# Performance work log

Measured on AMD Instinct MI355X. Metric: run time of the kernel, lower is better.

Reference implementation:

```python
import jax, jax.numpy as jnp
import numpy as np

B, T = 8, 16384
CLASSES, RC, EC = 256, 32, 256
NLAYERS = 40          # blocks(4) * layers(10)
DIL = 1024            # source uses 2**layers for every layer (faithful to code)
EPS = 1e-5


def _shift_right(x, d):
    # causal shift: y[t] = x[t-d], zero-padded
    return jnp.pad(x, ((0, 0), (0, 0), (d, 0)))[:, :, : x.shape[-1]]


def _conv1x1(x, w, b):
    # w: [out, in], x: [B, in, T]
    return jnp.einsum('oi,bit->bot', w, x) + b[None, :, None]


def _dconv2(x, w, b, d):
    # causal dilated conv, kernel 2: y[t] = w[:,:,0] x[t-d] + w[:,:,1] x[t] + b
    return (jnp.einsum('oi,bit->bot', w[:, :, 1], x)
            + jnp.einsum('oi,bit->bot', w[:, :, 0], _shift_right(x, d))
            + b[None, :, None])


def _bn(x, g, b):
    # training-mode BatchNorm1d: batch stats over (N, L)
    m = jnp.mean(x, axis=(0, 2), keepdims=True)
    v = jnp.var(x, axis=(0, 2), keepdims=True)
    return (x - m) * jax.lax.rsqrt(v + EPS) * g[None, :, None] + b[None, :, None]


def _mish(x):
    return x * jnp.tanh(jax.nn.softplus(x))


def setup_inputs() -> dict:
    key = jax.random.key(0)
    ks = jax.random.split(key, 16)
    n = jax.random.normal
    return {
        'x': n(ks[0], (B, CLASSES, T), jnp.float32),
        'start_w': n(ks[1], (RC, CLASSES), jnp.float32) * 0.05,
        'start_b': n(ks[2], (RC,), jnp.float32) * 0.05,
        'gt_w': n(ks[3], (NLAYERS, RC, RC, 2), jnp.float32) * 0.1,   # tanh branch
        'gt_b': n(ks[4], (NLAYERS, RC), jnp.float32) * 0.05,
        'gs_w': n(ks[5], (NLAYERS, RC, RC, 2), jnp.float32) * 0.1,   # sigmoid branch
        'gs_b': n(ks[6], (NLAYERS, RC), jnp.float32) * 0.05,
        'res_w': n(ks[7], (NLAYERS, RC, RC), jnp.float32) * 0.1,
        'res_b': n(ks[8], (NLAYERS, RC), jnp.float32) * 0.05,
        'bn_g': jnp.ones((NLAYERS, RC), jnp.float32),
        'bn_b': jnp.zeros((NLAYERS, RC), jnp.float32),
        'bn1_g': jnp.ones((RC,), jnp.float32),
        'bn1_b': jnp.zeros((RC,), jnp.float32),
        'e1_w': n(ks[9], (EC, RC), jnp.float32) * 0.1,
        'e1_b': n(ks[10], (EC,), jnp.float32) * 0.05,
        'bn2_g': jnp.ones((EC,), jnp.float32),
        'bn2_b': jnp.zeros((EC,), jnp.float32),
        'e2_w': n(ks[11], (CLASSES, EC), jnp.float32) * 0.05,
        'e2_b': n(ks[12], (CLASSES,), jnp.float32) * 0.05,
    }


def reference(x, start_w, start_b, gt_w, gt_b, gs_w, gs_b, res_w, res_b,
              bn_g, bn_b, bn1_g, bn1_b, e1_w, e1_b, bn2_g, bn2_b, e2_w, e2_b):
    # start_conv: CausalConv(classes, RC, k=1, shift=1) -> 1x1 conv on x shifted right by 1
    h = _conv1x1(_shift_right(x, 1), start_w, start_b)  # [B, RC, T]

    def step(carry, p):
        h, skip = carry
        gtw, gtb, gsw, gsb, rw, rb, bg, bb = p
        g = jnp.tanh(_dconv2(h, gtw, gtb, DIL)) * jax.nn.sigmoid(_dconv2(h, gsw, gsb, DIL))
        skip = skip + g
        h = h + _bn(_conv1x1(g, rw, rb), bg, bb)
        return (h, skip), None

    init = (h, jnp.zeros_like(h))
    (h, skip_sum), _ = jax.lax.scan(
        step, init, (gt_w, gt_b, gs_w, gs_b, res_w, res_b, bn_g, bn_b))

    y = _mish(_bn(skip_sum, bn1_g, bn1_b))
    y = _mish(_bn(_conv1x1(y, e1_w, e1_b), bn2_g, bn2_b))
    return _conv1x1(y, e2_w, e2_b)  # [B, CLASSES, T]
```

## Files before the change

kernel.cpp:

```cpp
#include <hip/hip_runtime.h>
#include <hip/hip_cooperative_groups.h>

namespace cg = cooperative_groups;


#define EPSV 1e-5f
#define RN   (1.f/131072.f)

#define H_OFF  0
#define SK_OFF (4*1024*1024)
#define ST_OFF (8*1024*1024)
#define ST_SKIP 2560
#define ST_MU   2624
#define ST_Y    2656
#define ST_A2   3680
#define ST_B2   3936
#define ST_TOT  4192
#define LST_N   (40*8*64)

__device__ __forceinline__ float rcp_f(float x) { return __builtin_amdgcn_rcpf(x); }
__device__ __forceinline__ float tanh_f(float x) {
    float e = __expf(2.f * x);
    return 1.f - 2.f * rcp_f(e + 1.f);
}
__device__ __forceinline__ float sigm_f(float x) { return rcp_f(1.f + __expf(-x)); }
__device__ __forceinline__ float mish_f(float x) {
    float e = __expf(x);
    float sp = (x > 15.f) ? x : __logf(1.f + e);
    return x * tanh_f(sp);
}

__global__ void k_zero(float* __restrict__ p, int n) {
    int i = blockIdx.x * 256 + threadIdx.x;
    if (i < n) p[i] = 0.f;
}

__global__ __launch_bounds__(256) void k_start(
        const float* __restrict__ x, const float* __restrict__ sw_g,
        const float* __restrict__ sb_g, float* __restrict__ h, float* __restrict__ skip)
{
    __shared__ float sw[256*36];
    __shared__ float sb[32];
    int tid = threadIdx.x, blk = blockIdx.x;
    int b = blk >> 6, r0 = (blk & 63) << 4;
    for (int k = tid; k < 8192; k += 256) {
        int o = k >> 8, c = k & 255;
        sw[c*36 + o] = sw_g[k];
    }
    if (tid < 32) sb[tid] = sb_g[tid];
    __syncthreads();

    int rr = tid & 15, s = tid >> 4;
    int t = r0 + rr + (s << 10);
    bool valid = (t >= 1);
    const float* xr = x + (long)b*256*16384 + (valid ? (t-1) : 0);
    float acc[32];
    #pragma unroll
    for (int o = 0; o < 32; ++o) acc[o] = 0.f;
    for (int c = 0; c < 256; ++c) {
        float xv = xr[(long)c*16384];
        xv = valid ? xv : 0.f;
        const float4* wrow = (const float4*)&sw[c*36];
        #pragma unroll
        for (int o4 = 0; o4 < 8; ++o4) {
            float4 w = wrow[o4];
            acc[o4*4+0] += w.x*xv; acc[o4*4+1] += w.y*xv;
            acc[o4*4+2] += w.z*xv; acc[o4*4+3] += w.w*xv;
        }
    }
    __syncthreads();
    #pragma unroll
    for (int o = 0; o < 32; ++o) sw[(rr*32 + o)*16 + s] = acc[o] + sb[o];
    __syncthreads();
    float4* hd = (float4*)(h + (long)blk*8192);
    float4* sd = (float4*)(skip + (long)blk*8192);
    const float4* ss = (const float4*)sw;
    float4 z4 = make_float4(0.f, 0.f, 0.f, 0.f);
    for (int k = tid; k < 2048; k += 256) { hd[k] = ss[k]; sd[k] = z4; }
}

__global__ __launch_bounds__(512, 4) void k_fused(
        const float* __restrict__ gt_w, const float* __restrict__ gt_b,
        const float* __restrict__ gs_w, const float* __restrict__ gs_b,
        const float* __restrict__ res_w, const float* __restrict__ res_b,
        const float* __restrict__ bn_g, const float* __restrict__ bn_b,
        const float* __restrict__ h, float* __restrict__ skip,
        float* __restrict__ st, float* __restrict__ lst)
{
    __shared__ float s_w[4096];
    __shared__ float s_r[1024];
    __shared__ float s_hg[8192];
    __shared__ float s_red[8][32][2];
    __shared__ float s_ab[64];

    int tid = threadIdx.x;
    int o = tid & 31, chl = tid >> 5;
    long base = (long)blockIdx.x*8192 + chl*512 + o*16;
    int slot = blockIdx.x & 7;

    float hreg[16], sk[16], zr[16];
    {
        const float4* hp4 = (const float4*)(h + base);
        #pragma unroll
        for (int q = 0; q < 4; ++q) {
            float4 t4 = hp4[q];
            hreg[4*q+0]=t4.x; hreg[4*q+1]=t4.y; hreg[4*q+2]=t4.z; hreg[4*q+3]=t4.w;
        }
    }
    #pragma unroll
    for (int s = 0; s < 16; ++s) sk[s] = 0.f;

    cg::grid_group grid = cg::this_grid();

    for (int L = 0; L < 40; ++L) {
        for (int k = tid; k < 1024; k += 512) {
            int oo = k >> 5, ii = k & 31;
            float2 a = ((const float2*)(gt_w + (long)L*2048))[k];
            float2 c = ((const float2*)(gs_w + (long)L*2048))[k];
            float* d = &s_w[(ii*32 + oo)*4];
            d[0] = a.x; d[1] = a.y; d[2] = c.x; d[3] = c.y;
            s_r[ii*32 + oo] = res_w[(long)L*1024 + k];
        }

        if (L > 0) {
            if (tid < 32) {
                float ssum = 0.f, ssq = 0.f;
                #pragma unroll
                for (int r = 0; r < 8; ++r) {
                    ssum += __hip_atomic_load(&lst[((L-1)*8 + r)*64 + tid],
                                              __ATOMIC_RELAXED, __HIP_MEMORY_SCOPE_AGENT);
                    ssq  += __hip_atomic_load(&lst[((L-1)*8 + r)*64 + 32 + tid],
                                              __ATOMIC_RELAXED, __HIP_MEMORY_SCOPE_AGENT);
                }
                float m = ssum * RN;
                float v = ssq * RN - m*m;
                float a = rsqrtf(v + EPSV) * bn_g[(L-1)*32 + tid];
                s_ab[tid] = a;
                s_ab[32 + tid] = bn_b[(L-1)*32 + tid] - m*a;
            }
            __syncthreads();
            float a = s_ab[o], bb = s_ab[32 + o];
            #pragma unroll
            for (int s = 0; s < 16; ++s) hreg[s] += zr[s]*a + bb;
        }

        float4* hs4 = (float4*)&s_hg[chl*512 + o*16];
        #pragma unroll
        for (int q = 0; q < 4; ++q)
            hs4[q] = make_float4(hreg[4*q], hreg[4*q+1], hreg[4*q+2], hreg[4*q+3]);
        __syncthreads();

        float aT[16], aS[16];
        float gtb = gt_b[L*32 + o], gsb = gs_b[L*32 + o];
        #pragma unroll
        for (int s = 0; s < 16; ++s) { aT[s] = gtb; aS[s] = gsb; }
        #pragma unroll 4
        for (int i = 0; i < 32; ++i) {
            float4 w = *(const float4*)&s_w[(i*32 + o)*4];
            const float4* hr = (const float4*)&s_hg[chl*512 + i*16];
            float hp = 0.f;
            #pragma unroll
            for (int s4 = 0; s4 < 4; ++s4) {
                float4 hv = hr[s4];
                int s = 4*s4;
                aT[s+0] += w.y*hv.x + w.x*hp;   aS[s+0] += w.w*hv.x + w.z*hp;
                aT[s+1] += w.y*hv.y + w.x*hv.x; aS[s+1] += w.w*hv.y + w.z*hv.x;
                aT[s+2] += w.y*hv.z + w.x*hv.y; aS[s+2] += w.w*hv.z + w.z*hv.y;
                aT[s+3] += w.y*hv.w + w.x*hv.z; aS[s+3] += w.w*hv.w + w.z*hv.z;
                hp = hv.w;
            }
        }
        float g[16];
        #pragma unroll
        for (int s = 0; s < 16; ++s) {
            g[s] = tanh_f(aT[s]) * sigm_f(aS[s]);
            sk[s] += g[s];
        }

        if (L < 39) {
            __syncthreads();
            #pragma unroll
            for (int q = 0; q < 4; ++q)
                hs4[q] = make_float4(g[4*q], g[4*q+1], g[4*q+2], g[4*q+3]);
            __syncthreads();

            float rbv = res_b[L*32 + o];
            #pragma unroll
            for (int s = 0; s < 16; ++s) zr[s] = rbv;
            #pragma unroll 4
            for (int i = 0; i < 32; ++i) {
                float w = s_r[i*32 + o];
                const float4* gr = (const float4*)&s_hg[chl*512 + i*16];
                #pragma unroll
                for (int s4 = 0; s4 < 4; ++s4) {
                    float4 gv = gr[s4];
                    zr[4*s4+0] += w*gv.x; zr[4*s4+1] += w*gv.y;
                    zr[4*s4+2] += w*gv.z; zr[4*s4+3] += w*gv.w;
                }
            }

            float ps = 0.f, pq = 0.f;
            #pragma unroll
            for (int s = 0; s < 16; ++s) { ps += zr[s]; pq += zr[s]*zr[s]; }
            ps += __shfl_down(ps, 32); pq += __shfl_down(pq, 32);
            int wv = tid >> 6;
            if ((tid & 63) < 32) { s_red[wv][o][0] = ps; s_red[wv][o][1] = pq; }
            __syncthreads();
            if (tid < 32) {
                float a = 0.f;
                #pragma unroll
                for (int w8 = 0; w8 < 8; ++w8) a += s_red[w8][tid][0];
                atomicAdd(&lst[(L*8 + slot)*64 + tid], a);
            } else if (tid < 64) {
                int c = tid - 32;
                float a = 0.f;
                #pragma unroll
                for (int w8 = 0; w8 < 8; ++w8) a += s_red[w8][c][1];
                atomicAdd(&lst[(L*8 + slot)*64 + 32 + c], a);
            }
            grid.sync();
        }
    }

    {
        float4* skp4 = (float4*)(skip + base);
        #pragma unroll
        for (int q = 0; q < 4; ++q)
            skp4[q] = make_float4(sk[4*q], sk[4*q+1], sk[4*q+2], sk[4*q+3]);

        float p2 = 0.f, q2 = 0.f;
        #pragma unroll
        for (int s = 0; s < 16; ++s) { p2 += sk[s]; q2 += sk[s]*sk[s]; }
        p2 += __shfl_down(p2, 32); q2 += __shfl_down(q2, 32);
        int wv = tid >> 6;
        __syncthreads();
        if ((tid & 63) < 32) { s_red[wv][o][0] = p2; s_red[wv][o][1] = q2; }
        __syncthreads();
        if (tid < 32) {
            float a = 0.f;
            #pragma unroll
            for (int w8 = 0; w8 < 8; ++w8) a += s_red[w8][tid][0];
            atomicAdd(&st[ST_SKIP + tid], a);
        } else if (tid < 64) {
            int c = tid - 32;
            float a = 0.f;
            #pragma unroll
            for (int w8 = 0; w8 < 8; ++w8) a += s_red[w8][c][1];
            atomicAdd(&st[ST_SKIP + 32 + c], a);
        }
    }
}

__global__ __launch_bounds__(256) void k_layer(
        const float* __restrict__ gt_w, const float* __restrict__ gt_b,
        const float* __restrict__ gs_w, const float* __restrict__ gs_b,
        const float* __restrict__ res_w, const float* __restrict__ res_b,
        const float* __restrict__ bn_g, const float* __restrict__ bn_b,
        float* __restrict__ h, float* __restrict__ z, float* __restrict__ skip,
        float* __restrict__ st, int L)
{
    __shared__ float s_w[4096];
    __shared__ float s_r[1024];
    __shared__ float s_hg[4096];
    __shared__ float s_red[4][32][2];

    int tid = threadIdx.x;
    int o = tid & 31, chl = tid >> 5;
    long base = (long)blockIdx.x*4096 + chl*512 + o*16;

    for (int k = tid; k < 1024; k += 256) {
        int oo = k >> 5, ii = k & 31;
        float2 a = ((const float2*)(gt_w + (long)L*2048))[k];
        float2 c = ((const float2*)(gs_w + (long)L*2048))[k];
        float* d = &s_w[(ii*32 + oo)*4];
        d[0] = a.x; d[1] = a.y; d[2] = c.x; d[3] = c.y;
        s_r[ii*32 + oo] = res_w[(long)L*1024 + k];
    }

    float hreg[16];
    float4* hp4 = (float4*)(h + base);
    #pragma unroll
    for (int q = 0; q < 4; ++q) {
        float4 t4 = hp4[q];
        hreg[4*q+0]=t4.x; hreg[4*q+1]=t4.y; hreg[4*q+2]=t4.z; hreg[4*q+3]=t4.w;
    }
    if (L > 0) {
        float ssum = st[(L-1)*64 + o], ssq = st[(L-1)*64 + 32 + o];
        float m = ssum * RN;
        float v = ssq * RN - m*m;
        float a = rsqrtf(v + EPSV) * bn_g[(L-1)*32 + o];
        float bb = bn_b[(L-1)*32 + o] - m*a;
        const float4* zp4 = (const float4*)(z + base);
        #pragma unroll
        for (int q = 0; q < 4; ++q) {
            float4 t4 = zp4[q];
            hreg[4*q+0] += t4.x*a + bb; hreg[4*q+1] += t4.y*a + bb;
            hreg[4*q+2] += t4.z*a + bb; hreg[4*q+3] += t4.w*a + bb;
        }
        #pragma unroll
        for (int q = 0; q < 4; ++q)
            hp4[q] = make_float4(hreg[4*q], hreg[4*q+1], hreg[4*q+2], hreg[4*q+3]);
    }
    float4* hs4 = (float4*)&s_hg[chl*512 + o*16];
    #pragma unroll
    for (int q = 0; q < 4; ++q)
        hs4[q] = make_float4(hreg[4*q], hreg[4*q+1], hreg[4*q+2], hreg[4*q+3]);
    __syncthreads();

    float aT[16], aS[16];
    float gtb = gt_b[L*32 + o], gsb = gs_b[L*32 + o];
    #pragma unroll
    for (int s = 0; s < 16; ++s) { aT[s] = gtb; aS[s] = gsb; }
    #pragma unroll 4
    for (int i = 0; i < 32; ++i) {
        float4 w = *(const float4*)&s_w[(i*32 + o)*4];
        const float4* hr = (const float4*)&s_hg[chl*512 + i*16];
        float hp = 0.f;
        #pragma unroll
        for (int s4 = 0; s4 < 4; ++s4) {
            float4 hv = hr[s4];
            int s = 4*s4;
            aT[s+0] += w.y*hv.x + w.x*hp;   aS[s+0] += w.w*hv.x + w.z*hp;
            aT[s+1] += w.y*hv.y + w.x*hv.x; aS[s+1] += w.w*hv.y + w.z*hv.x;
            aT[s+2] += w.y*hv.z + w.x*hv.y; aS[s+2] += w.w*hv.z + w.z*hv.y;
            aT[s+3] += w.y*hv.w + w.x*hv.z; aS[s+3] += w.w*hv.w + w.z*hv.z;
            hp = hv.w;
        }
    }
    float g[16], sk[16];
    #pragma unroll
    for (int s = 0; s < 16; ++s) g[s] = tanh_f(aT[s]) * sigm_f(aS[s]);

    float4* skp4 = (float4*)(skip + base);
    #pragma unroll
    for (int q = 0; q < 4; ++q) {
        float4 t4 = skp4[q];
        sk[4*q+0] = t4.x + g[4*q+0]; sk[4*q+1] = t4.y + g[4*q+1];
        sk[4*q+2] = t4.z + g[4*q+2]; sk[4*q+3] = t4.w + g[4*q+3];
        skp4[q] = make_float4(sk[4*q], sk[4*q+1], sk[4*q+2], sk[4*q+3]);
    }

    __syncthreads();
    #pragma unroll
    for (int q = 0; q < 4; ++q)
        hs4[q] = make_float4(g[4*q], g[4*q+1], g[4*q+2], g[4*q+3]);
    __syncthreads();

    float az[16];
    float rbv = res_b[L*32 + o];
    #pragma unroll
    for (int s = 0; s < 16; ++s) az[s] = rbv;
    #pragma unroll 4
    for (int i = 0; i < 32; ++i) {
        float w = s_r[i*32 + o];
        const float4* gr = (const float4*)&s_hg[chl*512 + i*16];
        #pragma unroll
        for (int s4 = 0; s4 < 4; ++s4) {
            float4 gv = gr[s4];
            az[4*s4+0] += w*gv.x; az[4*s4+1] += w*gv.y;
            az[4*s4+2] += w*gv.z; az[4*s4+3] += w*gv.w;
        }
    }
    float4* zp4w = (float4*)(z + base);
    #pragma unroll
    for (int q = 0; q < 4; ++q)
        zp4w[q] = make_float4(az[4*q], az[4*q+1], az[4*q+2], az[4*q+3]);

    float ps = 0.f, pq = 0.f;
    #pragma unroll
    for (int s = 0; s < 16; ++s) { ps += az[s]; pq += az[s]*az[s]; }
    ps += __shfl_down(ps, 32); pq += __shfl_down(pq, 32);
    int wv = tid >> 6;
    if ((tid & 63) < 32) { s_red[wv][o][0] = ps; s_red[wv][o][1] = pq; }
    __syncthreads();
    if (tid < 32) {
        float a = s_red[0][tid][0] + s_red[1][tid][0] + s_red[2][tid][0] + s_red[3][tid][0];
        atomicAdd(&st[L*64 + tid], a);
    } else if (tid < 64) {
        int c = tid - 32;
        float a = s_red[0][c][1] + s_red[1][c][1] + s_red[2][c][1] + s_red[3][c][1];
        atomicAdd(&st[L*64 + 32 + c], a);
    }

    if (L == 39) {
        float p2 = 0.f, q2 = 0.f;
        #pragma unroll
        for (int s = 0; s < 16; ++s) { p2 += sk[s]; q2 += sk[s]*sk[s]; }
        p2 += __shfl_down(p2, 32); q2 += __shfl_down(q2, 32);
        __syncthreads();
        if ((tid & 63) < 32) { s_red[wv][o][0] = p2; s_red[wv][o][1] = q2; }
        __syncthreads();
        if (tid < 32) {
            float a = s_red[0][tid][0] + s_red[1][tid][0] + s_red[2][tid][0] + s_red[3][tid][0];
            atomicAdd(&st[ST_SKIP + tid], a);
        } else if (tid < 64) {
            int c = tid - 32;
            float a = s_red[0][c][1] + s_red[1][c][1] + s_red[2][c][1] + s_red[3][c][1];
            atomicAdd(&st[ST_SKIP + 32 + c], a);
        }
    }
}

__global__ __launch_bounds__(256) void k_ep_a(
        const float* __restrict__ skip, const float* __restrict__ bn1_g,
        const float* __restrict__ bn1_b, float* __restrict__ st)
{
    __shared__ float sy[256*33];
    __shared__ float sA[32], sB[32];
    int tid = threadIdx.x;
    long cb = (long)blockIdx.x * 8192;
    if (tid < 32) {
        float ssum = st[ST_SKIP + tid], ssq = st[ST_SKIP + 32 + tid];
        float m = ssum * RN, v = ssq * RN - m*m;
        float a = rsqrtf(v + EPSV) * bn1_g[tid];
        sA[tid] = a; sB[tid] = bn1_b[tid] - m*a;
    }
    __syncthreads();
    for (int k = tid; k < 8192; k += 256) {
        int i = k & 31, p = k >> 5;
        int rr = p & 15, s = p >> 4;
        float v = skip[cb + rr*512 + i*16 + s];
        sy[p*33 + i] = mish_f(v * sA[i] + sB[i]);
    }
    __syncthreads();
    if (tid < 32) {
        float mu = 0.f;
        for (int p = 0; p < 256; ++p) mu += sy[p*33 + tid];
        atomicAdd(&st[ST_MU + tid], mu);
    }
    int jj = tid & 31, i0 = tid >> 5;
    float a0 = 0.f, a1 = 0.f, a2 = 0.f, a3 = 0.f;
    for (int p = 0; p < 256; ++p) {
        float yj = sy[p*33 + jj];
        a0 += yj * sy[p*33 + i0];
        a1 += yj * sy[p*33 + i0 + 8];
        a2 += yj * sy[p*33 + i0 + 16];
        a3 += yj * sy[p*33 + i0 + 24];
    }
    atomicAdd(&st[ST_Y + (i0     )*32 + jj], a0);
    atomicAdd(&st[ST_Y + (i0 +  8)*32 + jj], a1);
    atomicAdd(&st[ST_Y + (i0 + 16)*32 + jj], a2);
    atomicAdd(&st[ST_Y + (i0 + 24)*32 + jj], a3);
}

__global__ void k_ep_b(
        const float* __restrict__ e1_w, const float* __restrict__ e1_b,
        const float* __restrict__ bn2_g, const float* __restrict__ bn2_b,
        float* __restrict__ st)
{
    __shared__ float mu[32];
    int o = threadIdx.x;
    if (o < 32) mu[o] = st[ST_MU + o] * RN;
    __syncthreads();
    float w[32];
    const float4* wr = (const float4*)(e1_w + o*32);
    #pragma unroll
    for (int q = 0; q < 8; ++q) {
        float4 t4 = wr[q];
        w[4*q]=t4.x; w[4*q+1]=t4.y; w[4*q+2]=t4.z; w[4*q+3]=t4.w;
    }
    float m2 = e1_b[o];
    #pragma unroll
    for (int i = 0; i < 32; ++i) m2 += w[i]*mu[i];
    float var = 0.f;
    for (int i = 0; i < 32; ++i) {
        float wi = w[i], mi = mu[i];
        for (int j = 0; j < 32; ++j)
            var += wi * w[j] * (st[ST_Y + i*32 + j]*RN - mi*mu[j]);
    }
    float a2 = rsqrtf(var + EPSV) * bn2_g[o];
    st[ST_A2 + o] = a2;
    st[ST_B2 + o] = bn2_b[o] - m2*a2;
}

__global__ __launch_bounds__(256, 4) void k_ep_c(
        const float* __restrict__ skip,
        const float* __restrict__ bn1_g, const float* __restrict__ bn1_b,
        const float* __restrict__ e1_w, const float* __restrict__ e1_b,
        const float* __restrict__ e2_w, const float* __restrict__ e2_b,
        const float* __restrict__ st, float* __restrict__ out)
{
    __shared__ float y1l[32*32];
    __shared__ float y2l[256*36];
    int tid = threadIdx.x;
    int blk2 = blockIdx.x;
    int blk = blk2 >> 1, half = blk2 & 1;
    int b = blk >> 6, r0 = (blk & 63) << 4;
    long cb = (long)blk * 8192;
    float w1[32];
    {
        const float4* wr = (const float4*)(e1_w + tid*32);
        #pragma unroll
        for (int q = 0; q < 8; ++q) {
            float4 t4 = wr[q];
            w1[4*q]=t4.x; w1[4*q+1]=t4.y; w1[4*q+2]=t4.z; w1[4*q+3]=t4.w;
        }
    }
    float a2 = st[ST_A2 + tid], b2 = st[ST_B2 + tid];
    float eb1 = e1_b[tid];
    float eb2 = e2_b[tid];
    const float4* w2row = (const float4*)(e2_w + (long)tid * 256);

    for (int st8 = half*4; st8 < half*4 + 4; ++st8) {
        for (int k = tid; k < 1024; k += 256) {
            int i = k >> 5, q = k & 31;
            float ssum = st[ST_SKIP + i], ssq = st[ST_SKIP + 32 + i];
            float m = ssum * RN, vv = ssq * RN - m*m;
            float a1 = rsqrtf(vv + EPSV) * bn1_g[i];
            float b1 = bn1_b[i] - m*a1;
            int rr = q & 15, sl = q >> 4;
            float v = skip[cb + rr*512 + i*16 + st8*2 + sl];
            y1l[i*32 + q] = mish_f(v * a1 + b1);
        }
        __syncthreads();
        #pragma unroll 2
        for (int q4 = 0; q4 < 8; ++q4) {
            float4 acc = make_float4(eb1, eb1, eb1, eb1);
            #pragma unroll 8
            for (int i = 0; i < 32; ++i) {
                float4 yv = *(const float4*)&y1l[i*32 + q4*4];
                float wi = w1[i];
                acc.x += wi*yv.x; acc.y += wi*yv.y; acc.z += wi*yv.z; acc.w += wi*yv.w;
            }
            float4 y2v;
            y2v.x = mish_f(acc.x*a2 + b2);
            y2v.y = mish_f(acc.y*a2 + b2);
            y2v.z = mish_f(acc.z*a2 + b2);
            y2v.w = mish_f(acc.w*a2 + b2);
            *(float4*)&y2l[tid*36 + q4*4] = y2v;
        }
        __syncthreads();
        float acc[32];
        #pragma unroll
        for (int q = 0; q < 32; ++q) acc[q] = eb2;
        for (int i4 = 0; i4 < 64; ++i4) {
            float4 w4 = w2row[i4];
            float wa[4] = {w4.x, w4.y, w4.z, w4.w};
            #pragma unroll
            for (int ii = 0; ii < 4; ++ii) {
                float wv = wa[ii];
                const float* yr = &y2l[(i4*4 + ii)*36];
                #pragma unroll
                for (int q4 = 0; q4 < 8; ++q4) {
                    float4 yv = *(const float4*)&yr[q4*4];
                    acc[q4*4+0] += wv*yv.x; acc[q4*4+1] += wv*yv.y;
                    acc[q4*4+2] += wv*yv.z; acc[q4*4+3] += wv*yv.w;
                }
            }
        }
        long ob = ((long)b*256 + tid)*16384 + (long)(st8*2)*1024 + r0;
        float4* op = (float4*)&out[ob];
        op[0] = make_float4(acc[0],  acc[1],  acc[2],  acc[3]);
        op[1] = make_float4(acc[4],  acc[5],  acc[6],  acc[7]);
        op[2] = make_float4(acc[8],  acc[9],  acc[10], acc[11]);
        op[3] = make_float4(acc[12], acc[13], acc[14], acc[15]);
        float4* op2 = (float4*)&out[ob + 1024];
        op2[0] = make_float4(acc[16], acc[17], acc[18], acc[19]);
        op2[1] = make_float4(acc[20], acc[21], acc[22], acc[23]);
        op2[2] = make_float4(acc[24], acc[25], acc[26], acc[27]);
        op2[3] = make_float4(acc[28], acc[29], acc[30], acc[31]);
    }
}

extern "C" void kernel_launch(void* const* d_in, const int* in_sizes, int n_in,
                              void* d_out, int out_size, void* d_ws, size_t ws_size,
                              hipStream_t stream) {
    const float* x       = (const float*)d_in[0];
    const float* start_w = (const float*)d_in[1];
    const float* start_b = (const float*)d_in[2];
    const float* gt_w    = (const float*)d_in[3];
    const float* gt_b    = (const float*)d_in[4];
    const float* gs_w    = (const float*)d_in[5];
    const float* gs_b    = (const float*)d_in[6];
    const float* res_w   = (const float*)d_in[7];
    const float* res_b   = (const float*)d_in[8];
    const float* bn_g    = (const float*)d_in[9];
    const float* bn_b    = (const float*)d_in[10];
    const float* bn1_g   = (const float*)d_in[11];
    const float* bn1_b   = (const float*)d_in[12];
    const float* e1_w    = (const float*)d_in[13];
    const float* e1_b    = (const float*)d_in[14];
    const float* bn2_g   = (const float*)d_in[15];
    const float* bn2_b   = (const float*)d_in[16];
    const float* e2_w    = (const float*)d_in[17];
    const float* e2_b    = (const float*)d_in[18];
    float* ws  = (float*)d_ws;
    float* out = (float*)d_out;

    float* h    = ws + H_OFF;
    float* skip = ws + SK_OFF;
    float* st   = ws + ST_OFF;
    float* lst  = out;

    int coop_ok = 0;
    {
        int dev = 0, attr = 0, occ = 0;
        if (hipGetDevice(&dev) == hipSuccess &&
            hipDeviceGetAttribute(&attr, hipDeviceAttributeCooperativeLaunch, dev)
                == hipSuccess && attr) {
            if (hipOccupancyMaxActiveBlocksPerMultiprocessor(&occ, k_fused, 512, 0)
                    == hipSuccess && occ >= 2)
                coop_ok = 1;
        }
    }

    k_zero<<<dim3(17), dim3(256), 0, stream>>>(st, ST_TOT);
    k_zero<<<dim3(80), dim3(256), 0, stream>>>(lst, LST_N);
    k_start<<<dim3(512), dim3(256), 0, stream>>>(x, start_w, start_b, h, skip);

    if (coop_ok) {
        void* kargs[12] = {
            (void*)&gt_w, (void*)&gt_b, (void*)&gs_w, (void*)&gs_b,
            (void*)&res_w, (void*)&res_b, (void*)&bn_g, (void*)&bn_b,
            (void*)&h, (void*)&skip, (void*)&st, (void*)&lst };
        if (hipLaunchCooperativeKernel(k_fused, dim3(512), dim3(512),
                                       kargs, 0, stream) != hipSuccess)
            coop_ok = 0;
    }
    if (!coop_ok) {
        size_t need_full = ((size_t)ST_OFF + 8192 + 4*1024*1024) * 4;
        float* z = (ws_size >= need_full) ? (ws + ST_OFF + 8192)
                                          : (float*)d_out;
        for (int L = 0; L < 40; ++L)
            k_layer<<<dim3(1024), dim3(256), 0, stream>>>(
                gt_w, gt_b, gs_w, gs_b, res_w, res_b, bn_g, bn_b, h, z, skip, st, L);
    }

    k_ep_a<<<dim3(512), dim3(256), 0, stream>>>(skip, bn1_g, bn1_b, st);
    k_ep_b<<<dim3(1), dim3(256), 0, stream>>>(e1_w, e1_b, bn2_g, bn2_b, st);
    k_ep_c<<<dim3(1024), dim3(256), 0, stream>>>(skip, bn1_g, bn1_b, e1_w, e1_b,
                                                 e2_w, e2_b, st, out);
}
```

Baseline: 2.611 ms.

## Coarsen fused WaveNet kernel to two chunks per thread with swizzled LDS rows

```diff
diff --git a/kernel.cpp b/kernel.cpp
--- a/kernel.cpp
+++ b/kernel.cpp
@@ -79,7 +79,62 @@
     for (int k = tid; k < 2048; k += 256) { hd[k] = ss[k]; sd[k] = z4; }
 }
 
-__global__ __launch_bounds__(512, 4) void k_fused(
+__device__ __forceinline__ void stage16(float* __restrict__ row, int o,
+                                        const float* __restrict__ v) {
+    float4* p = (float4*)row;
+    int sw = (o >> 1) & 3;
+    p[0^sw] = make_float4(v[0],  v[1],  v[2],  v[3]);
+    p[1^sw] = make_float4(v[4],  v[5],  v[6],  v[7]);
+    p[2^sw] = make_float4(v[8],  v[9],  v[10], v[11]);
+    p[3^sw] = make_float4(v[12], v[13], v[14], v[15]);
+}
+
+__device__ __forceinline__ void gate_mv(const float* __restrict__ s_w,
+        const float* __restrict__ hg, int o, float gtb, float gsb,
+        float* __restrict__ aT, float* __restrict__ aS)
+{
+    #pragma unroll
+    for (int s = 0; s < 16; ++s) { aT[s] = gtb; aS[s] = gsb; }
+    #pragma unroll 4
+    for (int i = 0; i < 32; ++i) {
+        float4 w = *(const float4*)&s_w[(i*32 + o)*4];
+        const float4* hr = (const float4*)&hg[i*16];
+        int swi = (i >> 1) & 3;
+        float hv[16];
+        *(float4*)&hv[0]  = hr[0^swi];
+        *(float4*)&hv[4]  = hr[1^swi];
+        *(float4*)&hv[8]  = hr[2^swi];
+        *(float4*)&hv[12] = hr[3^swi];
+        aT[0] += w.y*hv[0];  aS[0] += w.w*hv[0];
+        #pragma unroll
+        for (int s = 1; s < 16; ++s) {
+            aT[s] += w.y*hv[s] + w.x*hv[s-1];
+            aS[s] += w.w*hv[s] + w.z*hv[s-1];
+        }
+    }
+}
+
+__device__ __forceinline__ void res_mv(const float* __restrict__ s_r,
+        const float* __restrict__ hg, int o, float rbv, float* __restrict__ zr)
+{
+    #pragma unroll
+    for (int s = 0; s < 16; ++s) zr[s] = rbv;
+    #pragma unroll 4
+    for (int i = 0; i < 32; ++i) {
+        float w = s_r[i*32 + o];
+        const float4* gr = (const float4*)&hg[i*16];
+        int swi = (i >> 1) & 3;
+        float gv[16];
+        *(float4*)&gv[0]  = gr[0^swi];
+        *(float4*)&gv[4]  = gr[1^swi];
+        *(float4*)&gv[8]  = gr[2^swi];
+        *(float4*)&gv[12] = gr[3^swi];
+        #pragma unroll
+        for (int s = 0; s < 16; ++s) zr[s] += w*gv[s];
+    }
+}
+
+__global__ __launch_bounds__(256, 2) void k_fused2(
         const float* __restrict__ gt_w, const float* __restrict__ gt_b,
         const float* __restrict__ gs_w, const float* __restrict__ gs_b,
         const float* __restrict__ res_w, const float* __restrict__ res_b,
@@ -90,30 +145,35 @@
     __shared__ float s_w[4096];
     __shared__ float s_r[1024];
     __shared__ float s_hg[8192];
-    __shared__ float s_red[8][32][2];
+    __shared__ float s_red[4][32][2];
     __shared__ float s_ab[64];
 
     int tid = threadIdx.x;
-    int o = tid & 31, chl = tid >> 5;
-    long base = (long)blockIdx.x*8192 + chl*512 + o*16;
+    int o = tid & 31, c0 = tid >> 5;
+    long baseA = (long)blockIdx.x*8192 + c0*512 + o*16;
+    long baseB = baseA + 8*512;
     int slot = blockIdx.x & 7;
-
-    float hreg[16], sk[16], zr[16];
+    float* rowA = &s_hg[c0*512 + o*16];
+    float* rowB = &s_hg[(c0+8)*512 + o*16];
+
+    float hA[16], hB[16], skA[16], skB[16], zrA[16], zrB[16];
     {
-        const float4* hp4 = (const float4*)(h + base);
+        const float4* pa = (const float4*)(h + baseA);
+        const float4* pb = (const float4*)(h + baseB);
         #pragma unroll
         for (int q = 0; q < 4; ++q) {
-            float4 t4 = hp4[q];
-            hreg[4*q+0]=t4.x; hreg[4*q+1]=t4.y; hreg[4*q+2]=t4.z; hreg[4*q+3]=t4.w;
-        }
-    }
-    #pragma unroll
-    for (int s = 0; s < 16; ++s) sk[s] = 0.f;
+            float4 ta = pa[q], tb = pb[q];
+            hA[4*q+0]=ta.x; hA[4*q+1]=ta.y; hA[4*q+2]=ta.z; hA[4*q+3]=ta.w;
+            hB[4*q+0]=tb.x; hB[4*q+1]=tb.y; hB[4*q+2]=tb.z; hB[4*q+3]=tb.w;
+        }
+    }
+    #pragma unroll
+    for (int s = 0; s < 16; ++s) { skA[s] = 0.f; skB[s] = 0.f; }
 
     cg::grid_group grid = cg::this_grid();
 
     for (int L = 0; L < 40; ++L) {
-        for (int k = tid; k < 1024; k += 512) {
+        for (int k = tid; k < 1024; k += 256) {
             int oo = k >> 5, ii = k & 31;
             float2 a = ((const float2*)(gt_w + (long)L*2048))[k];
             float2 c = ((const float2*)(gs_w + (long)L*2048))[k];
@@ -121,101 +181,78 @@
             d[0] = a.x; d[1] = a.y; d[2] = c.x; d[3] = c.y;
             s_r[ii*32 + oo] = res_w[(long)L*1024 + k];
         }
+        if (L > 0 && tid < 32) {
+            float ssum = 0.f, ssq = 0.f;
+            #pragma unroll
+            for (int r = 0; r < 8; ++r) {
+                ssum += __hip_atomic_load(&lst[((L-1)*8 + r)*64 + tid],
+                                          __ATOMIC_RELAXED, __HIP_MEMORY_SCOPE_AGENT);
+                ssq  += __hip_atomic_load(&lst[((L-1)*8 + r)*64 + 32 + tid],
+                                          __ATOMIC_RELAXED, __HIP_MEMORY_SCOPE_AGENT);
+            }
+            float m = ssum * RN;
+            float v = ssq * RN - m*m;
+            float a = rsqrtf(v + EPSV) * bn_g[(L-1)*32 + tid];
+            s_ab[tid] = a;
+            s_ab[32 + tid] = bn_b[(L-1)*32 + tid] - m*a;
+        }
+        __syncthreads();
 
         if (L > 0) {
-            if (tid < 32) {
-                float ssum = 0.f, ssq = 0.f;
-                #pragma unroll
-                for (int r = 0; r < 8; ++r) {
-                    ssum += __hip_atomic_load(&lst[((L-1)*8 + r)*64 + tid],
-                                              __ATOMIC_RELAXED, __HIP_MEMORY_SCOPE_AGENT);
-                    ssq  += __hip_atomic_load(&lst[((L-1)*8 + r)*64 + 32 + tid],
-                                              __ATOMIC_RELAXED, __HIP_MEMORY_SCOPE_AGENT);
-                }
-                float m = ssum * RN;
-                float v = ssq * RN - m*m;
-                float a = rsqrtf(v + EPSV) * bn_g[(L-1)*32 + tid];
-                s_ab[tid] = a;
-                s_ab[32 + tid] = bn_b[(L-1)*32 + tid] - m*a;
-            }
-            __syncthreads();
             float a = s_ab[o], bb = s_ab[32 + o];
             #pragma unroll
-            for (int s = 0; s < 16; ++s) hreg[s] += zr[s]*a + bb;
-        }
-
-        float4* hs4 = (float4*)&s_hg[chl*512 + o*16];
-        #pragma unroll
-        for (int q = 0; q < 4; ++q)
-            hs4[q] = make_float4(hreg[4*q], hreg[4*q+1], hreg[4*q+2], hreg[4*q+3]);
-        __syncthreads();
-
-        float aT[16], aS[16];
-        float gtb = gt_b[L*32 + o], gsb = gs_b[L*32 + o];
-        #pragma unroll
-        for (int s = 0; s < 16; ++s) { aT[s] = gtb; aS[s] = gsb; }
-        #pragma unroll 4
-        for (int i = 0; i < 32; ++i) {
-            float4 w = *(const float4*)&s_w[(i*32 + o)*4];
-            const float4* hr = (const float4*)&s_hg[chl*512 + i*16];
-            float hp = 0.f;
+            for (int s = 0; s < 16; ++s) {
+                hA[s] += zrA[s]*a + bb;
+                hB[s] += zrB[s]*a + bb;
+            }
+        }
+
+        stage16(rowA, o, hA);
+        stage16(rowB, o, hB);
+
+        float gA[16], gB[16];
+        {
+            float aT[16], aS[16];
+            float gtb = gt_b[L*32 + o], gsb = gs_b[L*32 + o];
+            gate_mv(s_w, &s_hg[c0*512], o, gtb, gsb, aT, aS);
             #pragma unroll
-            for (int s4 = 0; s4 < 4; ++s4) {
-                float4 hv = hr[s4];
-                int s = 4*s4;
-                aT[s+0] += w.y*hv.x + w.x*hp;   aS[s+0] += w.w*hv.x + w.z*hp;
-                aT[s+1] += w.y*hv.y + w.x*hv.x; aS[s+1] += w.w*hv.y + w.z*hv.x;
-                aT[s+2] += w.y*hv.z + w.x*hv.y; aS[s+2] += w.w*hv.z + w.z*hv.y;
-                aT[s+3] += w.y*hv.w + w.x*hv.z; aS[s+3] += w.w*hv.w + w.z*hv.z;
-                hp = hv.w;
-            }
-        }
-        float g[16];
-        #pragma unroll
-        for (int s = 0; s < 16; ++s) {
-            g[s] = tanh_f(aT[s]) * sigm_f(aS[s]);
-            sk[s] += g[s];
+            for (int s = 0; s < 16; ++s) {
+                gA[s] = tanh_f(aT[s]) * sigm_f(aS[s]);
+                skA[s] += gA[s];
+            }
+            gate_mv(s_w, &s_hg[(c0+8)*512], o, gtb, gsb, aT, aS);
+            #pragma unroll
+            for (int s = 0; s < 16; ++s) {
+                gB[s] = tanh_f(aT[s]) * sigm_f(aS[s]);
+                skB[s] += gB[s];
+            }
         }
 
         if (L < 39) {
-            __syncthreads();
-            #pragma unroll
-            for (int q = 0; q < 4; ++q)
-                hs4[q] = make_float4(g[4*q], g[4*q+1], g[4*q+2], g[4*q+3]);
-            __syncthreads();
-
+            stage16(rowA, o, gA);
+            stage16(rowB, o, gB);
             float rbv = res_b[L*32 + o];
-            #pragma unroll
-            for (int s = 0; s < 16; ++s) zr[s] = rbv;
-            #pragma unroll 4
-            for (int i = 0; i < 32; ++i) {
-                float w = s_r[i*32 + o];
-                const float4* gr = (const float4*)&s_hg[chl*512 + i*16];
-                #pragma unroll
-                for (int s4 = 0; s4 < 4; ++s4) {
-                    float4 gv = gr[s4];
-                    zr[4*s4+0] += w*gv.x; zr[4*s4+1] += w*gv.y;
-                    zr[4*s4+2] += w*gv.z; zr[4*s4+3] += w*gv.w;
-                }
-            }
+            res_mv(s_r, &s_hg[c0*512],     o, rbv, zrA);
+            res_mv(s_r, &s_hg[(c0+8)*512], o, rbv, zrB);
 
             float ps = 0.f, pq = 0.f;
             #pragma unroll
-            for (int s = 0; s < 16; ++s) { ps += zr[s]; pq += zr[s]*zr[s]; }
+            for (int s = 0; s < 16; ++s) {
+                ps += zrA[s] + zrB[s];
+                pq += zrA[s]*zrA[s] + zrB[s]*zrB[s];
+            }
             ps += __shfl_down(ps, 32); pq += __shfl_down(pq, 32);
             int wv = tid >> 6;
             if ((tid & 63) < 32) { s_red[wv][o][0] = ps; s_red[wv][o][1] = pq; }
             __syncthreads();
             if (tid < 32) {
-                float a = 0.f;
-                #pragma unroll
-                for (int w8 = 0; w8 < 8; ++w8) a += s_red[w8][tid][0];
+                float a = s_red[0][tid][0] + s_red[1][tid][0]
+                        + s_red[2][tid][0] + s_red[3][tid][0];
                 atomicAdd(&lst[(L*8 + slot)*64 + tid], a);
             } else if (tid < 64) {
                 int c = tid - 32;
-                float a = 0.f;
-                #pragma unroll
-                for (int w8 = 0; w8 < 8; ++w8) a += s_red[w8][c][1];
+                float a = s_red[0][c][1] + s_red[1][c][1]
+                        + s_red[2][c][1] + s_red[3][c][1];
                 atomicAdd(&lst[(L*8 + slot)*64 + 32 + c], a);
             }
             grid.sync();
@@ -223,29 +260,31 @@
     }
 
     {
-        float4* skp4 = (float4*)(skip + base);
-        #pragma unroll
-        for (int q = 0; q < 4; ++q)
-            skp4[q] = make_float4(sk[4*q], sk[4*q+1], sk[4*q+2], sk[4*q+3]);
-
+        float4* pa = (float4*)(skip + baseA);
+        float4* pb = (float4*)(skip + baseB);
+        #pragma unroll
+        for (int q = 0; q < 4; ++q) {
+            pa[q] = make_float4(skA[4*q], skA[4*q+1], skA[4*q+2], skA[4*q+3]);
+            pb[q] = make_float4(skB[4*q], skB[4*q+1], skB[4*q+2], skB[4*q+3]);
+        }
         float p2 = 0.f, q2 = 0.f;
         #pragma unroll
-        for (int s = 0; s < 16; ++s) { p2 += sk[s]; q2 += sk[s]*sk[s]; }
+        for (int s = 0; s < 16; ++s) {
+            p2 += skA[s] + skB[s];
+            q2 += skA[s]*skA[s] + skB[s]*skB[s];
+        }
         p2 += __shfl_down(p2, 32); q2 += __shfl_down(q2, 32);
         int wv = tid >> 6;
-        __syncthreads();
         if ((tid & 63) < 32) { s_red[wv][o][0] = p2; s_red[wv][o][1] = q2; }
         __syncthreads();
         if (tid < 32) {
-            float a = 0.f;
-            #pragma unroll
-            for (int w8 = 0; w8 < 8; ++w8) a += s_red[w8][tid][0];
+            float a = s_red[0][tid][0] + s_red[1][tid][0]
+                    + s_red[2][tid][0] + s_red[3][tid][0];
             atomicAdd(&st[ST_SKIP + tid], a);
         } else if (tid < 64) {
             int c = tid - 32;
-            float a = 0.f;
-            #pragma unroll
-            for (int w8 = 0; w8 < 8; ++w8) a += s_red[w8][c][1];
+            float a = s_red[0][c][1] + s_red[1][c][1]
+                    + s_red[2][c][1] + s_red[3][c][1];
             atomicAdd(&st[ST_SKIP + 32 + c], a);
         }
     }
@@ -598,7 +637,7 @@
         if (hipGetDevice(&dev) == hipSuccess &&
             hipDeviceGetAttribute(&attr, hipDeviceAttributeCooperativeLaunch, dev)
                 == hipSuccess && attr) {
-            if (hipOccupancyMaxActiveBlocksPerMultiprocessor(&occ, k_fused, 512, 0)
+            if (hipOccupancyMaxActiveBlocksPerMultiprocessor(&occ, k_fused2, 256, 0)
                     == hipSuccess && occ >= 2)
                 coop_ok = 1;
         }
@@ -613,7 +652,7 @@
             (void*)&gt_w, (void*)&gt_b, (void*)&gs_w, (void*)&gs_b,
             (void*)&res_w, (void*)&res_b, (void*)&bn_g, (void*)&bn_b,
             (void*)&h, (void*)&skip, (void*)&st, (void*)&lst };
-        if (hipLaunchCooperativeKernel(k_fused, dim3(512), dim3(512),
+        if (hipLaunchCooperativeKernel(k_fused2, dim3(512), dim3(256),
                                        kargs, 0, stream) != hipSuccess)
             coop_ok = 0;
     }
```

Result: no change. 2.595 ms (-0.6%).
